# Kernel tuning notes

Measured on AMD Instinct MI355X. Metric: run time of the kernel, lower is better.

## Reference

```python
import jax, jax.numpy as jnp
import numpy as np
from jax import lax

B, T = 1048576, 30

def setup_inputs() -> dict:
    key = jax.random.key(0)
    k = jax.random.split(key, 5)
    return {
        "x": jax.random.normal(k[0], (B, T, 1), dtype=jnp.float32),
        "W1": jax.random.normal(k[1], (T, 2, 20), dtype=jnp.float32) * 0.5,
        "b1": jax.random.normal(k[2], (T, 20), dtype=jnp.float32) * 0.1,
        "W2": jax.random.normal(k[3], (T, 20, 1), dtype=jnp.float32) * 0.5,
        "b2": jax.random.normal(k[4], (T, 1), dtype=jnp.float32) * 0.1,
    }

def reference(x, W1, b1, W2, b2):
    # x: [B, T, 1]; per-timestep MLP with recurrent concat of previous output.
    xt = jnp.transpose(x, (1, 0, 2))  # [T, B, 1]
    h0 = jnp.zeros((x.shape[0], 1), dtype=x.dtype)  # output_0

    def step(prev_out, inp):
        xi, w1, bb1, w2, bb2 = inp  # xi: [B,1], w1: [2,20], w2: [20,1]
        ih = jnp.concatenate([xi, prev_out], axis=1)       # [B, 2]
        h = jax.nn.relu(ih @ w1 + bb1)                     # [B, 20]
        o = jnp.tanh(h @ w2 + bb2)                         # [B, 1]
        return o, o

    _, outs = lax.scan(step, h0, (xt, W1, b1, W2, b2))  # outs: [T, B, 1]
    return jnp.transpose(outs, (1, 0, 2))  # [B, T, 1]
```

## Files before the change

### kernel.cpp

```cpp
#include <hip/hip_runtime.h>


#define TS  30
#define HID 20

typedef float f2 __attribute__((ext_vector_type(2)));

__device__ __forceinline__ float fast_tanh(float y) {
    float e = __expf(2.0f * y);
    return 1.0f - 2.0f * __builtin_amdgcn_rcpf(e + 1.0f);
}

__global__ __launch_bounds__(256) void rnn_fused(
        const float* __restrict__ x,
        const float* __restrict__ W1,
        const float* __restrict__ b1,
        const float* __restrict__ W2,
        const float* __restrict__ b2,
        float* __restrict__ out) {
    __shared__ float4 wt[TS * HID];
    __shared__ float  wb2[TS];

    const int tid = threadIdx.x;
    for (int i = tid; i < TS * HID; i += 256) {
        const int t = i / HID;
        const int j = i - t * HID;
        wt[i] = make_float4(W1[t * 40 + j], W1[t * 40 + 20 + j],
                            b1[t * 20 + j], W2[t * 20 + j]);
    }
    if (tid < TS) wb2[tid] = b2[tid];
    __syncthreads();

    const size_t e0 = (size_t)blockIdx.x * 1024 + (size_t)tid;
    const size_t e1 = e0 + 256;
    const size_t e2 = e0 + 512;
    const size_t e3 = e0 + 768;

    float r0[TS], r1[TS], r2[TS], r3[TS];
    {
        const float2* p0 = reinterpret_cast<const float2*>(x + e0 * TS);
        const float2* p1 = reinterpret_cast<const float2*>(x + e1 * TS);
        const float2* p2 = reinterpret_cast<const float2*>(x + e2 * TS);
        const float2* p3 = reinterpret_cast<const float2*>(x + e3 * TS);
#pragma unroll
        for (int i = 0; i < TS / 2; ++i) {
            float2 v;
            v = p0[i]; r0[2 * i] = v.x; r0[2 * i + 1] = v.y;
            v = p1[i]; r1[2 * i] = v.x; r1[2 * i + 1] = v.y;
            v = p2[i]; r2[2 * i] = v.x; r2[2 * i + 1] = v.y;
            v = p3[i]; r3[2 * i] = v.x; r3[2 * i + 1] = v.y;
        }
    }

    f2 oA = {0.0f, 0.0f};
    f2 oB = {0.0f, 0.0f};

#pragma unroll
    for (int t = 0; t < TS; ++t) {
        const float4* wrow = &wt[t * HID];
        const f2 xA = {r0[t], r1[t]};
        const f2 xB = {r2[t], r3[t]};
        const float bb = wb2[t];
        f2 accA = {bb, bb};
        f2 accB = {bb, bb};
#pragma unroll 4
        for (int j = 0; j < HID; ++j) {
            const float4 w = wrow[j];
            f2 hA = xA * w.x + oA * w.y + w.z;
            f2 hB = xB * w.x + oB * w.y + w.z;
            hA.x = __builtin_fmaxf(hA.x, 0.0f);
            hA.y = __builtin_fmaxf(hA.y, 0.0f);
            hB.x = __builtin_fmaxf(hB.x, 0.0f);
            hB.y = __builtin_fmaxf(hB.y, 0.0f);
            accA += hA * w.w;
            accB += hB * w.w;
        }
        oA.x = fast_tanh(accA.x);
        oA.y = fast_tanh(accA.y);
        oB.x = fast_tanh(accB.x);
        oB.y = fast_tanh(accB.y);
        r0[t] = oA.x; r1[t] = oA.y; r2[t] = oB.x; r3[t] = oB.y;
    }

    {
        float2* q0 = reinterpret_cast<float2*>(out + e0 * TS);
        float2* q1 = reinterpret_cast<float2*>(out + e1 * TS);
        float2* q2 = reinterpret_cast<float2*>(out + e2 * TS);
        float2* q3 = reinterpret_cast<float2*>(out + e3 * TS);
#pragma unroll
        for (int i = 0; i < TS / 2; ++i) {
            q0[i] = make_float2(r0[2 * i], r0[2 * i + 1]);
            q1[i] = make_float2(r1[2 * i], r1[2 * i + 1]);
            q2[i] = make_float2(r2[2 * i], r2[2 * i + 1]);
            q3[i] = make_float2(r3[2 * i], r3[2 * i + 1]);
        }
    }
}

extern "C" void kernel_launch(void* const* d_in, const int* in_sizes, int n_in,
                              void* d_out, int out_size, void* d_ws, size_t ws_size,
                              hipStream_t stream) {
    const float* x  = (const float*)d_in[0];
    const float* W1 = (const float*)d_in[1];
    const float* b1 = (const float*)d_in[2];
    const float* W2 = (const float*)d_in[3];
    const float* b2 = (const float*)d_in[4];
    float* out = (float*)d_out;

    const int B = 1048576;
    const int elems_per_block = 256 * 4;
    const int grid = B / elems_per_block;
    rnn_fused<<<grid, 256, 0, stream>>>(x, W1, b1, W2, b2, out);
}
```

Baseline: 311.7 us.

## Stage x through transposed shared tile and repack weights in a prep kernel

```diff
diff --git a/kernel.cpp b/kernel.cpp
--- a/kernel.cpp
+++ b/kernel.cpp
@@ -3,6 +3,9 @@
 
 #define TS  30
 #define HID 20
+#define THR 256
+#define EPB 512
+#define ROW 514
 
 typedef float f2 __attribute__((ext_vector_type(2)));
 
@@ -11,89 +14,81 @@
     return 1.0f - 2.0f * __builtin_amdgcn_rcpf(e + 1.0f);
 }
 
-__global__ __launch_bounds__(256) void rnn_fused(
+__global__ __launch_bounds__(256) void repack_w(
+        const float* __restrict__ W1, const float* __restrict__ b1,
+        const float* __restrict__ W2, const float* __restrict__ b2,
+        float4* __restrict__ wp) {
+    for (int i = threadIdx.x; i < TS * 21; i += 256) {
+        const int t = i / 21;
+        const int j = i - t * 21;
+        float4 v;
+        if (j < HID) v = make_float4(W1[t * 40 + j], W1[t * 40 + 20 + j],
+                                     b1[t * 20 + j], W2[t * 20 + j]);
+        else         v = make_float4(b2[t], 0.f, 0.f, 0.f);
+        wp[i] = v;
+    }
+}
+
+__global__ __launch_bounds__(256) void rnn2(
         const float* __restrict__ x,
-        const float* __restrict__ W1,
-        const float* __restrict__ b1,
-        const float* __restrict__ W2,
-        const float* __restrict__ b2,
+        const float4* __restrict__ wp,
         float* __restrict__ out) {
-    __shared__ float4 wt[TS * HID];
-    __shared__ float  wb2[TS];
+    __shared__ float tile[TS * ROW];
+    const int tid = threadIdx.x;
+    const size_t gbase = (size_t)blockIdx.x * (EPB * TS);
 
-    const int tid = threadIdx.x;
-    for (int i = tid; i < TS * HID; i += 256) {
-        const int t = i / HID;
-        const int j = i - t * HID;
-        wt[i] = make_float4(W1[t * 40 + j], W1[t * 40 + 20 + j],
-                            b1[t * 20 + j], W2[t * 20 + j]);
+    const float4* xg = reinterpret_cast<const float4*>(x + gbase);
+#pragma unroll
+    for (int i = 0; i < 15; ++i) {
+        float4 v = xg[i * THR + tid];
+        const unsigned fo = (unsigned)(i * THR + tid) * 4u;
+        const float* vp = reinterpret_cast<const float*>(&v);
+#pragma unroll
+        for (int k = 0; k < 4; ++k) {
+            const unsigned f = fo + k;
+            const unsigned e = (f * 34953u) >> 20;
+            const unsigned t = f - e * 30u;
+            tile[t * ROW + e] = vp[k];
+        }
     }
-    if (tid < TS) wb2[tid] = b2[tid];
     __syncthreads();
 
-    const size_t e0 = (size_t)blockIdx.x * 1024 + (size_t)tid;
-    const size_t e1 = e0 + 256;
-    const size_t e2 = e0 + 512;
-    const size_t e3 = e0 + 768;
+    f2 o = {0.f, 0.f};
+    const int e0 = 2 * tid;
+#pragma unroll 1
+    for (int t = 0; t < TS; ++t) {
+        const float4* wr = wp + t * 21;
+        const f2 xv = *reinterpret_cast<const f2*>(&tile[t * ROW + e0]);
+        const float bb = wr[20].x;
+        f2 acc = {bb, bb};
+#pragma unroll
+        for (int j = 0; j < HID; ++j) {
+            const float4 w = wr[j];
+            f2 h = xv * w.x + o * w.y + w.z;
+            h.x = __builtin_fmaxf(h.x, 0.f);
+            h.y = __builtin_fmaxf(h.y, 0.f);
+            acc += h * w.w;
+        }
+        o.x = fast_tanh(acc.x);
+        o.y = fast_tanh(acc.y);
+        *reinterpret_cast<f2*>(&tile[t * ROW + e0]) = o;
+    }
+    __syncthreads();
 
-    float r0[TS], r1[TS], r2[TS], r3[TS];
-    {
-        const float2* p0 = reinterpret_cast<const float2*>(x + e0 * TS);
-        const float2* p1 = reinterpret_cast<const float2*>(x + e1 * TS);
-        const float2* p2 = reinterpret_cast<const float2*>(x + e2 * TS);
-        const float2* p3 = reinterpret_cast<const float2*>(x + e3 * TS);
+    float4* og = reinterpret_cast<float4*>(out + gbase);
 #pragma unroll
-        for (int i = 0; i < TS / 2; ++i) {
-            float2 v;
-            v = p0[i]; r0[2 * i] = v.x; r0[2 * i + 1] = v.y;
-            v = p1[i]; r1[2 * i] = v.x; r1[2 * i + 1] = v.y;
-            v = p2[i]; r2[2 * i] = v.x; r2[2 * i + 1] = v.y;
-            v = p3[i]; r3[2 * i] = v.x; r3[2 * i + 1] = v.y;
+    for (int i = 0; i < 15; ++i) {
+        const unsigned fo = (unsigned)(i * THR + tid) * 4u;
+        float4 v;
+        float* vp = reinterpret_cast<float*>(&v);
+#pragma unroll
+        for (int k = 0; k < 4; ++k) {
+            const unsigned f = fo + k;
+            const unsigned e = (f * 34953u) >> 20;
+            const unsigned t = f - e * 30u;
+            vp[k] = tile[t * ROW + e];
         }
-    }
-
-    f2 oA = {0.0f, 0.0f};
-    f2 oB = {0.0f, 0.0f};
-
-#pragma unroll
-    for (int t = 0; t < TS; ++t) {
-        const float4* wrow = &wt[t * HID];
-        const f2 xA = {r0[t], r1[t]};
-        const f2 xB = {r2[t], r3[t]};
-        const float bb = wb2[t];
-        f2 accA = {bb, bb};
-        f2 accB = {bb, bb};
-#pragma unroll 4
-        for (int j = 0; j < HID; ++j) {
-            const float4 w = wrow[j];
-            f2 hA = xA * w.x + oA * w.y + w.z;
-            f2 hB = xB * w.x + oB * w.y + w.z;
-            hA.x = __builtin_fmaxf(hA.x, 0.0f);
-            hA.y = __builtin_fmaxf(hA.y, 0.0f);
-            hB.x = __builtin_fmaxf(hB.x, 0.0f);
-            hB.y = __builtin_fmaxf(hB.y, 0.0f);
-            accA += hA * w.w;
-            accB += hB * w.w;
-        }
-        oA.x = fast_tanh(accA.x);
-        oA.y = fast_tanh(accA.y);
-        oB.x = fast_tanh(accB.x);
-        oB.y = fast_tanh(accB.y);
-        r0[t] = oA.x; r1[t] = oA.y; r2[t] = oB.x; r3[t] = oB.y;
-    }
-
-    {
-        float2* q0 = reinterpret_cast<float2*>(out + e0 * TS);
-        float2* q1 = reinterpret_cast<float2*>(out + e1 * TS);
-        float2* q2 = reinterpret_cast<float2*>(out + e2 * TS);
-        float2* q3 = reinterpret_cast<float2*>(out + e3 * TS);
-#pragma unroll
-        for (int i = 0; i < TS / 2; ++i) {
-            q0[i] = make_float2(r0[2 * i], r0[2 * i + 1]);
-            q1[i] = make_float2(r1[2 * i], r1[2 * i + 1]);
-            q2[i] = make_float2(r2[2 * i], r2[2 * i + 1]);
-            q3[i] = make_float2(r3[2 * i], r3[2 * i + 1]);
-        }
+        og[i * THR + tid] = v;
     }
 }
 
@@ -106,9 +101,11 @@
     const float* W2 = (const float*)d_in[3];
     const float* b2 = (const float*)d_in[4];
     float* out = (float*)d_out;
+    float4* wp = (float4*)d_ws;
+
+    repack_w<<<1, 256, 0, stream>>>(W1, b1, W2, b2, wp);
 
     const int B = 1048576;
-    const int elems_per_block = 256 * 4;
-    const int grid = B / elems_per_block;
-    rnn_fused<<<grid, 256, 0, stream>>>(x, W1, b1, W2, b2, out);
+    const int grid = B / EPB;
+    rnn2<<<grid, 256, 0, stream>>>(x, wp, out);
 }
```

Result: faster. 266.6 us (-14.5%).
